# Optimization experiments

Hardware: AMD Instinct MI355X
Metric: run time of the kernel (lower is better)

Reference implementation:

```python
import jax, jax.numpy as jnp
import numpy as np

N_ATOMS = 50000
N_NBRS = 32
R_CUTOFF = 5.0
N_BASIS = 128
N_FILTERS = 128
N_GAUSS = 25
MAX_Z = 100
MEAN = 0.0
STDDEV = 20.0


def ssp(x):
    # shifted softplus: softplus(x) - log(2)
    return jax.nn.softplus(x) - jnp.log(2.0)


def setup_inputs() -> dict:
    key = jax.random.key(0)
    ks = jax.random.split(key, 18)
    dR = jax.random.uniform(ks[0], (N_ATOMS, N_NBRS), dtype=jnp.float32) * R_CUTOFF
    Z = jax.random.randint(ks[1], (N_ATOMS,), 0, MAX_Z)
    nbr_idx = jax.random.randint(ks[2], (N_ATOMS, N_NBRS), 0, N_ATOMS)

    def p(k, shape):
        fan_in = shape[0]
        return (jax.random.normal(k, shape, dtype=jnp.float32) / np.sqrt(fan_in)).astype(jnp.float32)

    return dict(
        dR=dR, Z=Z, nbr_idx=nbr_idx,
        embed_table=jax.random.normal(ks[3], (MAX_Z, N_BASIS), dtype=jnp.float32),
        fw1=p(ks[4], (N_GAUSS, N_FILTERS)), fb1=jnp.zeros((N_FILTERS,), jnp.float32),
        fw2=p(ks[5], (N_FILTERS, N_FILTERS)), fb2=jnp.zeros((N_FILTERS,), jnp.float32),
        in2f_w=p(ks[6], (N_BASIS, N_FILTERS)),
        f2out_w1=p(ks[7], (N_FILTERS, N_BASIS)), f2out_b1=jnp.zeros((N_BASIS,), jnp.float32),
        f2out_w2=p(ks[8], (N_BASIS, N_BASIS)), f2out_b2=jnp.zeros((N_BASIS,), jnp.float32),
        mlp_w1=p(ks[9], (N_BASIS, 64)), mlp_b1=jnp.zeros((64,), jnp.float32),
        mlp_w2=p(ks[10], (64, 1)), mlp_b2=jnp.zeros((1,), jnp.float32),
    )


def reference(dR, Z, nbr_idx, embed_table, fw1, fb1, fw2, fb2, in2f_w,
              f2out_w1, f2out_b1, f2out_w2, f2out_b2,
              mlp_w1, mlp_b1, mlp_w2, mlp_b2):
    # embedding lookup: [N, B]
    x = embed_table[Z]

    # gaussian smearing of distances: [N, K, G]
    offsets = jnp.linspace(0.0, R_CUTOFF, N_GAUSS, dtype=jnp.float32)
    coeff = -0.5 / (offsets[1] - offsets[0]) ** 2
    dr_exp = jnp.exp(coeff * (dR[..., None] - offsets) ** 2)

    # filter network: Dense+ssp, Dense -> [N, K, F]
    W = ssp(jnp.einsum('nkg,gf->nkf', dr_exp, fw1) + fb1)
    W = jnp.einsum('nkf,fh->nkh', W, fw2) + fb2

    # cosine cutoff
    fcut = 0.5 * (jnp.cos(dR * jnp.pi / R_CUTOFF) + 1.0) * (dR < R_CUTOFF)
    W = W * fcut[..., None]

    # cfconv: in2f (no bias), neighbor gather, elementwise filter, sum over neighbors
    y = x @ in2f_w                    # [N, F]
    y_nbrs = y[nbr_idx]               # [N, K, F] irregular gather
    mask = (nbr_idx < N_ATOMS)[..., None]
    agg = jnp.sum(jnp.where(mask, y_nbrs * W, 0.0), axis=1)  # [N, F]

    # f2out: Dense+ssp, Dense
    v = ssp(agg @ f2out_w1 + f2out_b1) @ f2out_w2 + f2out_b2

    # residual update
    x = x + v

    # atomwise MLP [128 -> 64 -> 1] with ssp between layers
    yi = ssp(x @ mlp_w1 + mlp_b1) @ mlp_w2 + mlp_b2  # [N, 1]
    yi = yi * STDDEV + MEAN

    # aggregate (sum over atom axis), per_atom=False
    return jnp.sum(yi, axis=0)  # [1]
```

## Files before the change

kernel.cpp:

```cpp
#include <hip/hip_runtime.h>
#include <math.h>

#define N_ATOMS  50000
#define N_NBRS   32
#define N_GAUSS  25
#define RCUT     5.0f
#define TT       192
#define TROWS    32
#define NTB      6
#define MAXZ     100
#define NT32     1563
#define ABLOCKS  512
#define NTILES   (N_ATOMS / 16)
#define DBLOCKS  1024
#define PI_F     3.14159265358979323846f

typedef unsigned int   uint_t;
typedef unsigned short ushort_t;
typedef _Float16 f16;
typedef f16   f16x2 __attribute__((ext_vector_type(2)));
typedef f16   f16x4 __attribute__((ext_vector_type(4)));
typedef f16   f16x8 __attribute__((ext_vector_type(8)));
typedef float f32x4 __attribute__((ext_vector_type(4)));

__device__ __forceinline__ float ssp(float x) {
  return fmaxf(x, 0.0f) + __logf(fmaf(0.5f, __expf(-fabsf(x)), 0.5f));
}
__device__ __forceinline__ f16x2 bch(uint_t u) {
  return __builtin_bit_cast(f16x2, u);
}
__device__ __forceinline__ uint_t hcb(f16x2 v) {
  return __builtin_bit_cast(uint_t, v);
}
__device__ __forceinline__ int swz(int m, int e) {
  return m * 128 + ((((e >> 3) ^ m) & 15) << 3) + (e & 7);
}

__global__ void __launch_bounds__(256, 2)
prep_all_kernel(const float* __restrict__ fw1,
                const float* __restrict__ fb1,
                const float* __restrict__ fw2,
                const float* __restrict__ fb2,
                const float* __restrict__ w1,
                const float* __restrict__ w2,
                const float* __restrict__ mw1,
                const float* __restrict__ embed,
                const float* __restrict__ in2f,
                f16* __restrict__ tabh,
                f16* __restrict__ ytab,
                f16* __restrict__ w1ht,
                f16* __restrict__ w2ht,
                f16* __restrict__ mw1ht) {
  const int tid = threadIdx.x;
  const int bid = blockIdx.x;

  __shared__ float sW2[128 * 128];
  __shared__ float sH[TROWS][128];

  if (bid < NTB) {
    const int i0 = bid * TROWS;
    #pragma unroll
    for (int t = 0; t < 16; ++t) {
      const int e = tid + t * 256;
      ((float4*)sW2)[e] = ((const float4*)fw2)[e];
    }
    {
      const int f  = tid & 127;
      const int rh = (tid >> 7) * (TROWS / 2);
      const float delta = RCUT / (float)(N_GAUSS - 1);
      const float coeff = -0.5f / (delta * delta);
      const float b1v = fb1[f];
      for (int j = 0; j < TROWS / 2; ++j) {
        const float r = (float)(i0 + rh + j) * (RCUT / 191.0f);
        float h = b1v;
        #pragma unroll
        for (int g = 0; g < N_GAUSS; ++g) {
          const float d = r - (float)g * delta;
          h = fmaf(__expf(coeff * d * d), fw1[g * 128 + f], h);
        }
        sH[rh + j][f] = ssp(h);
      }
    }
    __syncthreads();
    {
      const int c0 = (tid & 31) * 4;
      const int rg = (tid >> 5) * 4;
      f32x4 acc[4];
      const float4 bv = *(const float4*)&fb2[c0];
      #pragma unroll
      for (int j = 0; j < 4; ++j) acc[j] = (f32x4){bv.x, bv.y, bv.z, bv.w};
      for (int k = 0; k < 128; ++k) {
        const float4 wv = *(const float4*)&sW2[k * 128 + c0];
        #pragma unroll
        for (int j = 0; j < 4; ++j) {
          const float hv = sH[rg + j][k];
          acc[j][0] = fmaf(hv, wv.x, acc[j][0]);
          acc[j][1] = fmaf(hv, wv.y, acc[j][1]);
          acc[j][2] = fmaf(hv, wv.z, acc[j][2]);
          acc[j][3] = fmaf(hv, wv.w, acc[j][3]);
        }
      }
      #pragma unroll
      for (int j = 0; j < 4; ++j) {
        const int i = i0 + rg + j;
        const float r = (float)i * (RCUT / 191.0f);
        const float fc = (r < RCUT) ? 0.5f * (__cosf(r * PI_F / RCUT) + 1.0f) : 0.0f;
        f16x4 o;
        #pragma unroll
        for (int c = 0; c < 4; ++c) o[c] = (f16)(acc[j][c] * fc);
        *(f16x4*)&tabh[i * 128 + c0] = o;
      }
    }
  } else {
    const int cc = (bid - NTB) * 2 + (tid >> 7);
    const int i  = tid & 127;
    w1ht[cc * 128 + i] = (f16)w1[i * 128 + cc];
    w2ht[cc * 128 + i] = (f16)w2[i * 128 + cc];
    if (cc < 64) mw1ht[cc * 128 + i] = (f16)mw1[i * 64 + cc];
    float* xs = &sH[0][0] + (tid >> 7) * 128;
    xs[i] = (cc < MAXZ) ? embed[cc * 128 + i] : 0.0f;
    __syncthreads();
    if (cc < MAXZ) {
      float acc = 0.0f;
      for (int j = 0; j < 128; j += 4) {
        const float4 xv = *reinterpret_cast<const float4*>(&xs[j]);
        acc = fmaf(xv.x, in2f[(j + 0) * 128 + i], acc);
        acc = fmaf(xv.y, in2f[(j + 1) * 128 + i], acc);
        acc = fmaf(xv.z, in2f[(j + 2) * 128 + i], acc);
        acc = fmaf(xv.w, in2f[(j + 3) * 128 + i], acc);
      }
      ytab[cc * 128 + i] = (f16)acc;
    }
  }
}

__global__ void __launch_bounds__(512, 4)
cfconv_kernel(const float* __restrict__ dR,
              const int* __restrict__ Z,
              const int* __restrict__ nbr,
              const f16* __restrict__ tabh,
              const f16* __restrict__ ytab,
              f16* __restrict__ agg) {
  const int tid = threadIdx.x;
  __shared__ __align__(16) f16    sW[TT * 128];
  __shared__ __align__(16) f16    sYT[MAXZ * 128];
  __shared__ __align__(16) uint_t s_pk[1024];

  for (int e = tid; e < TT * 16; e += 512)   ((uint4*)sW)[e]  = ((const uint4*)tabh)[e];
  for (int e = tid; e < MAXZ * 16; e += 512) ((uint4*)sYT)[e] = ((const uint4*)ytab)[e];

  const int w  = tid >> 6;
  const int l  = tid & 63;
  const int q  = l >> 4;
  const int cq = l & 15;
  const int m  = w * 4 + q;
  const char* wb = (const char*)sW  + cq * 16;
  const char* yb = (const char*)sYT + cq * 16;

  for (int tile = blockIdx.x; tile < NT32; tile += ABLOCKS) {
    const int a0 = tile * 32;
    __syncthreads();
    #pragma unroll
    for (int t0 = 0; t0 < 2; ++t0) {
      const int t = tid + t0 * 512;
      const int pidx = a0 * N_NBRS + t;
      if (pidx < N_ATOMS * N_NBRS) {
        const float r = dR[pidx];
        const int  nb = nbr[pidx];
        int i0 = (int)(r * (191.0f / RCUT) + 0.5f);
        i0 = min(i0, 191);
        s_pk[t] = (uint_t)i0 | ((uint_t)Z[nb] << 8);
      }
    }
    __syncthreads();

    const int a = a0 + m;
    if (a < N_ATOMS) {
      f16x2 acc[4];
      #pragma unroll
      for (int c = 0; c < 4; ++c) acc[c] = (f16x2)0;

      uint4 twA[4], ytA[4], twB[4], ytB[4];

#define IG(BK, g) { \
    _Pragma("unroll") \
    for (int d = 0; d < 4; ++d) { \
      const uint_t pk = s_pk[m * N_NBRS + (g) * 4 + d]; \
      tw##BK[d] = *(const uint4*)(wb + ((pk & 0xFFu) << 8)); \
      yt##BK[d] = *(const uint4*)(yb + ((pk >> 8) << 8)); \
    } }

#define CG(BK) { \
    _Pragma("unroll") \
    for (int d = 0; d < 4; ++d) { \
      acc[0] += bch(tw##BK[d].x) * bch(yt##BK[d].x); \
      acc[1] += bch(tw##BK[d].y) * bch(yt##BK[d].y); \
      acc[2] += bch(tw##BK[d].z) * bch(yt##BK[d].z); \
      acc[3] += bch(tw##BK[d].w) * bch(yt##BK[d].w); \
    } }

      IG(A, 0) IG(B, 1)
      CG(A) IG(A, 2)
      CG(B) IG(B, 3)
      CG(A) IG(A, 4)
      CG(B) IG(B, 5)
      CG(A) IG(A, 6)
      CG(B) IG(B, 7)
      CG(A)
      CG(B)
#undef IG
#undef CG

      uint4 o;
      o.x = hcb(acc[0]); o.y = hcb(acc[1]); o.z = hcb(acc[2]); o.w = hcb(acc[3]);
      *(uint4*)&agg[(size_t)a * 128 + cq * 8] = o;
    }
  }
}

__global__ void __launch_bounds__(256, 3)
dense_kernel(const int* __restrict__ Z,
             const float* __restrict__ embed,
             const f16* __restrict__ agg,
             const f16* __restrict__ w1ht, const float* __restrict__ b1,
             const f16* __restrict__ w2ht, const float* __restrict__ b2,
             const f16* __restrict__ mw1ht, const float* __restrict__ mb1,
             const float* __restrict__ mw2,
             float* __restrict__ partial) {
  const int tid = threadIdx.x;
  const int wv  = tid >> 6;
  const int l   = tid & 63;
  const int rc  = l & 15;
  const int qk  = l >> 4;
  __shared__ __align__(16) f16 sA[16 * 128];
  __shared__ __align__(16) f16 sB[16 * 128];
  __shared__ int   sZ[16];
  __shared__ float sRed[4];

  f16x8 bw1[2][4], bw2[2][4], bwm[4];
  float bb1[2], bb2[2];
  #pragma unroll
  for (int t = 0; t < 2; ++t) {
    const int c = wv * 32 + t * 16 + rc;
    bb1[t] = b1[c];
    bb2[t] = b2[c];
    #pragma unroll
    for (int k0i = 0; k0i < 4; ++k0i) {
      bw1[t][k0i] = *(const f16x8*)&w1ht[c * 128 + k0i * 32 + qk * 8];
      bw2[t][k0i] = *(const f16x8*)&w2ht[c * 128 + k0i * 32 + qk * 8];
    }
  }
  const int c1 = wv * 16 + rc;
  #pragma unroll
  for (int k0i = 0; k0i < 4; ++k0i) {
    bwm[k0i] = *(const f16x8*)&mw1ht[c1 * 128 + k0i * 32 + qk * 8];
  }
  const float bm = mb1[c1];
  const float cm = mw2[c1];

  float vsum = 0.0f;

#define AFRAG(SRC, k0) (*(const f16x8*)&SRC[rc * 128 + (((((k0) >> 3) + qk) ^ rc) & 15) * 8])

  for (int tile = blockIdx.x; tile < NTILES; tile += DBLOCKS) {
    const int a0 = tile * 16;
    __syncthreads();

    {
      const int mm = tid >> 4, cc = tid & 15;
      const uint4 v = ((const uint4*)agg)[a0 * 16 + tid];
      *(uint4*)&sA[mm * 128 + (((cc ^ mm) & 15) << 3)] = v;
    }
    if (tid < 16) sZ[tid] = Z[a0 + tid];
    __syncthreads();

    f32x4 dacc[2];
    #pragma unroll
    for (int t = 0; t < 2; ++t) dacc[t] = (f32x4){bb1[t], bb1[t], bb1[t], bb1[t]};
    #pragma unroll
    for (int k0i = 0; k0i < 4; ++k0i) {
      const f16x8 af = AFRAG(sA, k0i * 32);
      #pragma unroll
      for (int t = 0; t < 2; ++t)
        dacc[t] = __builtin_amdgcn_mfma_f32_16x16x32_f16(af, bw1[t][k0i], dacc[t], 0, 0, 0);
    }
    #pragma unroll
    for (int t = 0; t < 2; ++t) {
      const int c = wv * 32 + t * 16 + rc;
      #pragma unroll
      for (int r = 0; r < 4; ++r) sB[swz(qk * 4 + r, c)] = (f16)ssp(dacc[t][r]);
    }
    __syncthreads();

    #pragma unroll
    for (int t = 0; t < 2; ++t) dacc[t] = (f32x4){bb2[t], bb2[t], bb2[t], bb2[t]};
    #pragma unroll
    for (int k0i = 0; k0i < 4; ++k0i) {
      const f16x8 af = AFRAG(sB, k0i * 32);
      #pragma unroll
      for (int t = 0; t < 2; ++t)
        dacc[t] = __builtin_amdgcn_mfma_f32_16x16x32_f16(af, bw2[t][k0i], dacc[t], 0, 0, 0);
    }
    #pragma unroll
    for (int t = 0; t < 2; ++t) {
      const int c = wv * 32 + t * 16 + rc;
      #pragma unroll
      for (int r = 0; r < 4; ++r) {
        const int mm = qk * 4 + r;
        const float x = embed[(size_t)sZ[mm] * 128 + c] + dacc[t][r];
        sA[swz(mm, c)] = (f16)x;
      }
    }
    __syncthreads();

    f32x4 a2 = (f32x4){bm, bm, bm, bm};
    #pragma unroll
    for (int k0i = 0; k0i < 4; ++k0i)
      a2 = __builtin_amdgcn_mfma_f32_16x16x32_f16(AFRAG(sA, k0i * 32), bwm[k0i], a2, 0, 0, 0);
    #pragma unroll
    for (int r = 0; r < 4; ++r) vsum = fmaf(ssp(a2[r]), cm, vsum);
  }
#undef AFRAG

  #pragma unroll
  for (int o = 1; o < 64; o <<= 1) vsum += __shfl_xor(vsum, o, 64);
  if (l == 0) sRed[wv] = vsum;
  __syncthreads();
  if (tid == 0) {
    partial[blockIdx.x] = sRed[0] + sRed[1] + sRed[2] + sRed[3];
  }
}

__global__ void __launch_bounds__(256, 1)
reduce_kernel(const float* __restrict__ partial,
              const float* __restrict__ mb2,
              float* __restrict__ out) {
  const int tid = threadIdx.x;
  float s = 0.0f;
  for (int i = tid; i < DBLOCKS; i += 256) s += partial[i];
  __shared__ float sr[4];
  #pragma unroll
  for (int o = 1; o < 64; o <<= 1) s += __shfl_xor(s, o, 64);
  if ((tid & 63) == 0) sr[tid >> 6] = s;
  __syncthreads();
  if (tid == 0) {
    out[0] = 20.0f * (sr[0] + sr[1] + sr[2] + sr[3] + (float)N_ATOMS * mb2[0]);
  }
}

extern "C" void kernel_launch(void* const* d_in, const int* in_sizes, int n_in,
                              void* d_out, int out_size, void* d_ws, size_t ws_size,
                              hipStream_t stream) {
  const float* dR    = (const float*)d_in[0];
  const int*   Z     = (const int*)  d_in[1];
  const int*   nbr   = (const int*)  d_in[2];
  const float* embed = (const float*)d_in[3];
  const float* fw1   = (const float*)d_in[4];
  const float* fb1   = (const float*)d_in[5];
  const float* fw2   = (const float*)d_in[6];
  const float* fb2   = (const float*)d_in[7];
  const float* in2f  = (const float*)d_in[8];
  const float* w1    = (const float*)d_in[9];
  const float* b1    = (const float*)d_in[10];
  const float* w2    = (const float*)d_in[11];
  const float* b2    = (const float*)d_in[12];
  const float* mw1   = (const float*)d_in[13];
  const float* mb1   = (const float*)d_in[14];
  const float* mw2   = (const float*)d_in[15];
  const float* mb2   = (const float*)d_in[16];
  float* out = (float*)d_out;

  char* ws = (char*)d_ws;
  f16*   tabh    = (f16*)ws;
  f16*   ytab    = (f16*)(ws + (size_t)64 * 1024);
  f16*   w1ht    = (f16*)(ws + (size_t)128 * 1024);
  f16*   w2ht    = (f16*)(ws + (size_t)192 * 1024);
  f16*   mw1ht   = (f16*)(ws + (size_t)256 * 1024);
  float* partial = (float*)(ws + (size_t)384 * 1024);
  f16*   agg     = (f16*)(ws + (size_t)512 * 1024);

  prep_all_kernel<<<NTB + 64, 256, 0, stream>>>(fw1, fb1, fw2, fb2,
      w1, w2, mw1, embed, in2f, tabh, ytab, w1ht, w2ht, mw1ht);
  cfconv_kernel<<<ABLOCKS, 512, 0, stream>>>(dR, Z, nbr, tabh, ytab, agg);
  dense_kernel<<<DBLOCKS, 256, 0, stream>>>(Z, embed, agg,
      w1ht, b1, w2ht, b2, mw1ht, mb1, mw2, partial);
  reduce_kernel<<<1, 256, 0, stream>>>(partial, mb2, out);
}
```

Baseline: 61.12 us.

## Fuse cfconv aggregation and dense MLP stages into one persistent kernel

Merges the neighbor-filter aggregation kernel and the dense f2out/MLP kernel into a single kernel. Each 512-thread block computes aggregates for 32 atoms straight into shared memory, then runs the MFMA dense chain on two 16-atom groups. This removes the fp16 agg round-trip through global memory and one kernel launch. In exchange, fewer blocks are launched (256) with lower occupancy, and the gather and MFMA phases are serialized within each block.

```diff
diff --git a/kernel.cpp b/kernel.cpp
--- a/kernel.cpp
+++ b/kernel.cpp
@@ -10,9 +10,7 @@
 #define NTB      6
 #define MAXZ     100
 #define NT32     1563
-#define ABLOCKS  512
-#define NTILES   (N_ATOMS / 16)
-#define DBLOCKS  1024
+#define PBLOCKS  256
 #define PI_F     3.14159265358979323846f
 
 typedef unsigned int   uint_t;
@@ -134,58 +132,100 @@
   }
 }
 
-__global__ void __launch_bounds__(512, 4)
-cfconv_kernel(const float* __restrict__ dR,
-              const int* __restrict__ Z,
-              const int* __restrict__ nbr,
-              const f16* __restrict__ tabh,
-              const f16* __restrict__ ytab,
-              f16* __restrict__ agg) {
+__global__ void __launch_bounds__(512, 2)
+fused_kernel(const float* __restrict__ dR,
+             const int* __restrict__ Z,
+             const int* __restrict__ nbr,
+             const float* __restrict__ embed,
+             const f16* __restrict__ tabh,
+             const f16* __restrict__ ytab,
+             const f16* __restrict__ w1ht, const float* __restrict__ b1,
+             const f16* __restrict__ w2ht, const float* __restrict__ b2,
+             const f16* __restrict__ mw1ht, const float* __restrict__ mb1,
+             const float* __restrict__ mw2,
+             float* __restrict__ partial) {
   const int tid = threadIdx.x;
+  const int w   = tid >> 6;
+  const int l   = tid & 63;
+  const int q   = l >> 4;
+  const int cq  = l & 15;
   __shared__ __align__(16) f16    sW[TT * 128];
   __shared__ __align__(16) f16    sYT[MAXZ * 128];
   __shared__ __align__(16) uint_t s_pk[1024];
+  __shared__ __align__(16) f16    sA[2][16 * 128];
+  __shared__ __align__(16) f16    sB[2][16 * 128];
+  __shared__ int   sZ[32];
+  __shared__ float sRed[8];
 
   for (int e = tid; e < TT * 16; e += 512)   ((uint4*)sW)[e]  = ((const uint4*)tabh)[e];
   for (int e = tid; e < MAXZ * 16; e += 512) ((uint4*)sYT)[e] = ((const uint4*)ytab)[e];
 
-  const int w  = tid >> 6;
-  const int l  = tid & 63;
-  const int q  = l >> 4;
-  const int cq = l & 15;
-  const int m  = w * 4 + q;
+  const int g   = w >> 2;
+  const int wvg = w & 3;
+  const int rc  = cq;
+  const int qk  = q;
+  f16x8 bw1[2][4], bw2[2][4], bwm[4];
+  float bb1[2], bb2[2];
+  #pragma unroll
+  for (int t = 0; t < 2; ++t) {
+    const int c = wvg * 32 + t * 16 + rc;
+    bb1[t] = b1[c];
+    bb2[t] = b2[c];
+    #pragma unroll
+    for (int k0i = 0; k0i < 4; ++k0i) {
+      bw1[t][k0i] = *(const f16x8*)&w1ht[c * 128 + k0i * 32 + qk * 8];
+      bw2[t][k0i] = *(const f16x8*)&w2ht[c * 128 + k0i * 32 + qk * 8];
+    }
+  }
+  const int c1 = wvg * 16 + rc;
+  #pragma unroll
+  for (int k0i = 0; k0i < 4; ++k0i) {
+    bwm[k0i] = *(const f16x8*)&mw1ht[c1 * 128 + k0i * 32 + qk * 8];
+  }
+  const float bm = mb1[c1];
+  const float cm = mw2[c1];
+
+  const int m = w * 4 + q;
   const char* wb = (const char*)sW  + cq * 16;
   const char* yb = (const char*)sYT + cq * 16;
 
-  for (int tile = blockIdx.x; tile < NT32; tile += ABLOCKS) {
-    const int a0 = tile * 32;
-    __syncthreads();
+  float vsum = 0.0f;
+  __syncthreads();
+
+#define AFRAG(SRC, k0) (*(const f16x8*)&SRC[rc * 128 + (((((k0) >> 3) + qk) ^ rc) & 15) * 8])
+
+  for (int chunk = blockIdx.x; chunk < NT32; chunk += PBLOCKS) {
+    const int a0 = chunk * 32;
+    __syncthreads();
+
     #pragma unroll
     for (int t0 = 0; t0 < 2; ++t0) {
       const int t = tid + t0 * 512;
       const int pidx = a0 * N_NBRS + t;
+      uint_t pk = 0;
       if (pidx < N_ATOMS * N_NBRS) {
         const float r = dR[pidx];
         const int  nb = nbr[pidx];
         int i0 = (int)(r * (191.0f / RCUT) + 0.5f);
         i0 = min(i0, 191);
-        s_pk[t] = (uint_t)i0 | ((uint_t)Z[nb] << 8);
-      }
-    }
-    __syncthreads();
-
-    const int a = a0 + m;
-    if (a < N_ATOMS) {
+        pk = (uint_t)i0 | ((uint_t)Z[nb] << 8);
+      }
+      s_pk[t] = pk;
+    }
+    if (tid < 32) sZ[tid] = (a0 + tid < N_ATOMS) ? Z[a0 + tid] : 0;
+    __syncthreads();
+
+    {
       f16x2 acc[4];
       #pragma unroll
       for (int c = 0; c < 4; ++c) acc[c] = (f16x2)0;
 
       uint4 twA[4], ytA[4], twB[4], ytB[4];
 
-#define IG(BK, g) { \
+#define IG(BK, gi) { \
     _Pragma("unroll") \
     for (int d = 0; d < 4; ++d) { \
-      const uint_t pk = s_pk[m * N_NBRS + (g) * 4 + d]; \
+      const uint_t pk = s_pk[m * N_NBRS + (gi) * 4 + d]; \
       tw##BK[d] = *(const uint4*)(wb + ((pk & 0xFFu) << 8)); \
       yt##BK[d] = *(const uint4*)(yb + ((pk >> 8) << 8)); \
     } }
@@ -213,82 +253,26 @@
 
       uint4 o;
       o.x = hcb(acc[0]); o.y = hcb(acc[1]); o.z = hcb(acc[2]); o.w = hcb(acc[3]);
-      *(uint4*)&agg[(size_t)a * 128 + cq * 8] = o;
-    }
-  }
-}
-
-__global__ void __launch_bounds__(256, 3)
-dense_kernel(const int* __restrict__ Z,
-             const float* __restrict__ embed,
-             const f16* __restrict__ agg,
-             const f16* __restrict__ w1ht, const float* __restrict__ b1,
-             const f16* __restrict__ w2ht, const float* __restrict__ b2,
-             const f16* __restrict__ mw1ht, const float* __restrict__ mb1,
-             const float* __restrict__ mw2,
-             float* __restrict__ partial) {
-  const int tid = threadIdx.x;
-  const int wv  = tid >> 6;
-  const int l   = tid & 63;
-  const int rc  = l & 15;
-  const int qk  = l >> 4;
-  __shared__ __align__(16) f16 sA[16 * 128];
-  __shared__ __align__(16) f16 sB[16 * 128];
-  __shared__ int   sZ[16];
-  __shared__ float sRed[4];
-
-  f16x8 bw1[2][4], bw2[2][4], bwm[4];
-  float bb1[2], bb2[2];
-  #pragma unroll
-  for (int t = 0; t < 2; ++t) {
-    const int c = wv * 32 + t * 16 + rc;
-    bb1[t] = b1[c];
-    bb2[t] = b2[c];
+      const int mm = m & 15;
+      *(uint4*)&sA[m >> 4][mm * 128 + (((cq ^ mm) & 15) << 3)] = o;
+    }
+    __syncthreads();
+
+    f32x4 dacc[2];
+    #pragma unroll
+    for (int t = 0; t < 2; ++t) dacc[t] = (f32x4){bb1[t], bb1[t], bb1[t], bb1[t]};
     #pragma unroll
     for (int k0i = 0; k0i < 4; ++k0i) {
-      bw1[t][k0i] = *(const f16x8*)&w1ht[c * 128 + k0i * 32 + qk * 8];
-      bw2[t][k0i] = *(const f16x8*)&w2ht[c * 128 + k0i * 32 + qk * 8];
-    }
-  }
-  const int c1 = wv * 16 + rc;
-  #pragma unroll
-  for (int k0i = 0; k0i < 4; ++k0i) {
-    bwm[k0i] = *(const f16x8*)&mw1ht[c1 * 128 + k0i * 32 + qk * 8];
-  }
-  const float bm = mb1[c1];
-  const float cm = mw2[c1];
-
-  float vsum = 0.0f;
-
-#define AFRAG(SRC, k0) (*(const f16x8*)&SRC[rc * 128 + (((((k0) >> 3) + qk) ^ rc) & 15) * 8])
-
-  for (int tile = blockIdx.x; tile < NTILES; tile += DBLOCKS) {
-    const int a0 = tile * 16;
-    __syncthreads();
-
-    {
-      const int mm = tid >> 4, cc = tid & 15;
-      const uint4 v = ((const uint4*)agg)[a0 * 16 + tid];
-      *(uint4*)&sA[mm * 128 + (((cc ^ mm) & 15) << 3)] = v;
-    }
-    if (tid < 16) sZ[tid] = Z[a0 + tid];
-    __syncthreads();
-
-    f32x4 dacc[2];
-    #pragma unroll
-    for (int t = 0; t < 2; ++t) dacc[t] = (f32x4){bb1[t], bb1[t], bb1[t], bb1[t]};
-    #pragma unroll
-    for (int k0i = 0; k0i < 4; ++k0i) {
-      const f16x8 af = AFRAG(sA, k0i * 32);
+      const f16x8 af = AFRAG(sA[g], k0i * 32);
       #pragma unroll
       for (int t = 0; t < 2; ++t)
         dacc[t] = __builtin_amdgcn_mfma_f32_16x16x32_f16(af, bw1[t][k0i], dacc[t], 0, 0, 0);
     }
     #pragma unroll
     for (int t = 0; t < 2; ++t) {
-      const int c = wv * 32 + t * 16 + rc;
-      #pragma unroll
-      for (int r = 0; r < 4; ++r) sB[swz(qk * 4 + r, c)] = (f16)ssp(dacc[t][r]);
+      const int c = wvg * 32 + t * 16 + rc;
+      #pragma unroll
+      for (int r = 0; r < 4; ++r) sB[g][swz(qk * 4 + r, c)] = (f16)ssp(dacc[t][r]);
     }
     __syncthreads();
 
@@ -296,19 +280,19 @@
     for (int t = 0; t < 2; ++t) dacc[t] = (f32x4){bb2[t], bb2[t], bb2[t], bb2[t]};
     #pragma unroll
     for (int k0i = 0; k0i < 4; ++k0i) {
-      const f16x8 af = AFRAG(sB, k0i * 32);
+      const f16x8 af = AFRAG(sB[g], k0i * 32);
       #pragma unroll
       for (int t = 0; t < 2; ++t)
         dacc[t] = __builtin_amdgcn_mfma_f32_16x16x32_f16(af, bw2[t][k0i], dacc[t], 0, 0, 0);
     }
     #pragma unroll
     for (int t = 0; t < 2; ++t) {
-      const int c = wv * 32 + t * 16 + rc;
+      const int c = wvg * 32 + t * 16 + rc;
       #pragma unroll
       for (int r = 0; r < 4; ++r) {
         const int mm = qk * 4 + r;
-        const float x = embed[(size_t)sZ[mm] * 128 + c] + dacc[t][r];
-        sA[swz(mm, c)] = (f16)x;
+        const float x = embed[(size_t)sZ[g * 16 + mm] * 128 + c] + dacc[t][r];
+        sA[g][swz(mm, c)] = (f16)x;
       }
     }
     __syncthreads();
@@ -316,18 +300,24 @@
     f32x4 a2 = (f32x4){bm, bm, bm, bm};
     #pragma unroll
     for (int k0i = 0; k0i < 4; ++k0i)
-      a2 = __builtin_amdgcn_mfma_f32_16x16x32_f16(AFRAG(sA, k0i * 32), bwm[k0i], a2, 0, 0, 0);
-    #pragma unroll
-    for (int r = 0; r < 4; ++r) vsum = fmaf(ssp(a2[r]), cm, vsum);
+      a2 = __builtin_amdgcn_mfma_f32_16x16x32_f16(AFRAG(sA[g], k0i * 32), bwm[k0i], a2, 0, 0, 0);
+    #pragma unroll
+    for (int r = 0; r < 4; ++r) {
+      const int atom = a0 + g * 16 + qk * 4 + r;
+      if (atom < N_ATOMS) vsum = fmaf(ssp(a2[r]), cm, vsum);
+    }
   }
 #undef AFRAG
 
   #pragma unroll
   for (int o = 1; o < 64; o <<= 1) vsum += __shfl_xor(vsum, o, 64);
-  if (l == 0) sRed[wv] = vsum;
+  if (l == 0) sRed[w] = vsum;
   __syncthreads();
   if (tid == 0) {
-    partial[blockIdx.x] = sRed[0] + sRed[1] + sRed[2] + sRed[3];
+    float s = 0.0f;
+    #pragma unroll
+    for (int i = 0; i < 8; ++i) s += sRed[i];
+    partial[blockIdx.x] = s;
   }
 }
 
@@ -336,8 +326,7 @@
               const float* __restrict__ mb2,
               float* __restrict__ out) {
   const int tid = threadIdx.x;
-  float s = 0.0f;
-  for (int i = tid; i < DBLOCKS; i += 256) s += partial[i];
+  float s = (tid < PBLOCKS) ? partial[tid] : 0.0f;
   __shared__ float sr[4];
   #pragma unroll
   for (int o = 1; o < 64; o <<= 1) s += __shfl_xor(s, o, 64);
@@ -377,12 +366,10 @@
   f16*   w2ht    = (f16*)(ws + (size_t)192 * 1024);
   f16*   mw1ht   = (f16*)(ws + (size_t)256 * 1024);
   float* partial = (float*)(ws + (size_t)384 * 1024);
-  f16*   agg     = (f16*)(ws + (size_t)512 * 1024);
 
   prep_all_kernel<<<NTB + 64, 256, 0, stream>>>(fw1, fb1, fw2, fb2,
       w1, w2, mw1, embed, in2f, tabh, ytab, w1ht, w2ht, mw1ht);
-  cfconv_kernel<<<ABLOCKS, 512, 0, stream>>>(dR, Z, nbr, tabh, ytab, agg);
-  dense_kernel<<<DBLOCKS, 256, 0, stream>>>(Z, embed, agg,
-      w1ht, b1, w2ht, b2, mw1ht, mb1, mw2, partial);
+  fused_kernel<<<PBLOCKS, 512, 0, stream>>>(dR, Z, nbr, embed,
+      tabh, ytab, w1ht, b1, w2ht, b2, mw1ht, mb1, mw2, partial);
   reduce_kernel<<<1, 256, 0, stream>>>(partial, mb2, out);
 }
```

Result: faster. 55.64 us (-9.0%).
